# Kernel tuning notes

Hardware: AMD Instinct MI355X
Metric: run time of the kernel (lower is better)

## Reference

```python
import jax, jax.numpy as jnp
import numpy as np

N, E, IN, HID, OUT = 50000, 800000, 128, 96, 2


def setup_inputs() -> dict:
    key = jax.random.key(0)
    ks = jax.random.split(key, 10)
    x = jax.random.normal(ks[0], (N, IN), jnp.float32)
    edge_index = jax.random.randint(ks[1], (2, E), 0, N, dtype=jnp.int64)
    # PQVA mask: per-node, first output channel is a "known" quantity (masked out),
    # second is the prediction target -> ~mask selects exactly N elements.
    m = np.zeros((N, OUT), dtype=bool)
    m[:, 0] = True
    PQVA_mask = jnp.asarray(m)
    scaler_mean = 0.1 * jax.random.normal(ks[2], (IN,), jnp.float32)
    scaler_std = 0.5 + jax.random.uniform(ks[3], (IN,), jnp.float32)  # in [0.5, 1.5)
    W1 = jax.random.normal(ks[4], (IN, HID), jnp.float32) / np.sqrt(IN)
    W2 = jax.random.normal(ks[5], (HID, HID), jnp.float32) / np.sqrt(HID)
    W3 = jax.random.normal(ks[6], (HID, HID), jnp.float32) / np.sqrt(HID)
    Wout = jax.random.normal(ks[7], (HID, OUT), jnp.float32) / np.sqrt(HID)
    b1 = jnp.zeros((HID,), jnp.float32)
    b2 = jnp.zeros((HID,), jnp.float32)
    b3 = jnp.zeros((HID,), jnp.float32)
    bout = jnp.zeros((OUT,), jnp.float32)
    return {"x": x, "edge_index": edge_index, "PQVA_mask": PQVA_mask,
            "scaler_mean": scaler_mean, "scaler_std": scaler_std,
            "W1": W1, "b1": b1, "W2": W2, "b2": b2, "W3": W3, "b3": b3,
            "Wout": Wout, "bout": bout}


def reference(x, edge_index, PQVA_mask, scaler_mean, scaler_std,
              W1, b1, W2, b2, W3, b3, Wout, bout):
    n = x.shape[0]
    loop = jnp.arange(n, dtype=edge_index.dtype)
    src = jnp.concatenate([edge_index[0], loop])  # add self-loops (GCNConv default)
    dst = jnp.concatenate([edge_index[1], loop])
    deg = jax.ops.segment_sum(jnp.ones_like(dst, x.dtype), dst, num_segments=n)
    dinv = jax.lax.rsqrt(deg)  # deg >= 1 thanks to self-loops
    norm = (dinv[src] * dinv[dst])[:, None]  # [E+N, 1]

    def prop(h):  # D^-1/2 (A+I) D^-1/2 @ h  via gather-scale-scatter
        return jax.ops.segment_sum(h[src] * norm, dst, num_segments=n)

    h = (x - scaler_mean) / scaler_std          # standard scaler
    h = jax.nn.relu(prop(h @ W1) + b1)          # GCNConv 1 + ReLU
    h = jax.nn.relu(prop(h @ W2) + b2)          # GCNConv 2 + ReLU
    h = prop(h @ W3) + b3                       # GCNConv 3 (last, no act)
    out = h @ Wout + bout                       # final Linear -> [N, OUT]
    # masked reshape: ~mask has exactly one True per node -> [N]
    return out.reshape(-1)[~PQVA_mask.reshape(-1)]
```

## Files before the change

### kernel.cpp

```cpp
#include <hip/hip_runtime.h>
#include <hip/hip_fp16.h>

#define IN_F 128
#define HID_F 96
#define PB 512
#define STRIDE 6144
#define MAXB 8192

typedef _Float16 f16x8 __attribute__((ext_vector_type(8)));
typedef float f32x4 __attribute__((ext_vector_type(4)));

__device__ __forceinline__ void swizzle_one(const float* W, __half* Wsw, int idx) {
    int j  = idx & 7;
    int ln = (idx >> 3) & 63;
    int ct = idx >> 9;
    int t = ct % 6, c = ct / 6;
    int k   = c * 32 + (ln >> 4) * 8 + j;
    int col = t * 16 + (ln & 15);
    Wsw[idx] = (__half)W[k * 96 + col];
}


__global__ __launch_bounds__(256) void part_prep_kernel(
        const int* __restrict__ srcv, const int* __restrict__ dstv,
        int* __restrict__ bcur, int* __restrict__ ebuf, int E,
        const float* __restrict__ stdv, float* __restrict__ rstd,
        const float* __restrict__ W3, const float* __restrict__ Wout,
        const float* __restrict__ b3, const float* __restrict__ bout,
        float* __restrict__ wv, float* __restrict__ cconst,
        const float* __restrict__ W1, __half* __restrict__ Wsw1, int SW1,
        const float* __restrict__ W2, __half* __restrict__ Wsw2, int SW2) {
    int b = blockIdx.x, t = threadIdx.x;
    if (b >= PB) {
        int pb = b - PB;
        if (pb == 0) {
            if (t < IN_F) rstd[t] = 1.0f / stdv[t];
            if (t < HID_F) {
                float s = 0.f;
                for (int j = 0; j < HID_F; ++j) s += W3[t * HID_F + j] * Wout[j * 2 + 1];
                wv[t] = s;
            }
            if (t == 0) {
                float s = 0.f;
                for (int j = 0; j < HID_F; ++j) s += b3[j] * Wout[j * 2 + 1];
                cconst[0] = s + bout[1];
            }
        } else if (pb <= 48) {
            int idx = (pb - 1) * 256 + t;
            if (idx < SW1) swizzle_one(W1, Wsw1, idx);
        } else {
            int idx = (pb - 49) * 256 + t;
            if (idx < SW2) swizzle_one(W2, Wsw2, idx);
        }
        return;
    }
    __shared__ int h[256];
    __shared__ int cur[256];
    int chunk = (E + PB - 1) / PB;
    int s = b * chunk;
    int eend = min(s + chunk, E);
    h[t] = 0;
    __syncthreads();
    for (int e = s + t; e < eend; e += 256) atomicAdd(&h[dstv[e] >> 8], 1);
    __syncthreads();
    if (h[t]) cur[t] = t * STRIDE + atomicAdd(&bcur[t], h[t]);
    __syncthreads();
    for (int e = s + t; e < eend; e += 256) {
        int sv = srcv[e], d = dstv[e];
        int p = atomicAdd(&cur[d >> 8], 1);
        ebuf[p] = (sv << 8) | (d & 255);
    }
}


__global__ __launch_bounds__(256) void buildcsr_kernel(
        const int* __restrict__ ebuf, const int* __restrict__ bcur,
        int* __restrict__ rowdeg, float* __restrict__ dinv,
        int* __restrict__ cols, int n) {
    __shared__ int dg[256];
    __shared__ int tmp[256];
    __shared__ int cur[256];
    __shared__ int colst[MAXB];
    int t = threadIdx.x;
    int k = blockIdx.x;
    int seg = k * STRIDE;
    int cnt = min(bcur[k], STRIDE);
    dg[t] = 0;
    __syncthreads();
    for (int i = t; i < cnt; i += 256) atomicAdd(&dg[ebuf[seg + i] & 255], 1);
    __syncthreads();
    int v = dg[t];
    tmp[t] = v;
    __syncthreads();
#pragma unroll
    for (int off = 1; off < 256; off <<= 1) {
        int u = (t >= off) ? tmp[t - off] : 0;
        __syncthreads();
        tmp[t] += u;
        __syncthreads();
    }
    int excl = tmp[t] - v;
    int node = (k << 8) + t;
    if (node < n) {
        rowdeg[node] = ((seg + excl) << 9) | v;
        dinv[node] = rsqrtf((float)v + 1.0f);
    }
    cur[t] = excl;
    __syncthreads();
    for (int i = t; i < cnt; i += 256) {
        int p = ebuf[seg + i];
        int lp = atomicAdd(&cur[p & 255], 1);
        colst[lp] = ((unsigned)p) >> 8;
    }
    __syncthreads();
    for (int i = t; i < cnt; i += 256) cols[seg + i] = colst[i];
}


template<int MODE, int K>
__global__ __launch_bounds__(256) void gemm_mfma_kernel(
        const void* __restrict__ Ain, const __half* __restrict__ Wsw,
        const float* __restrict__ mean, const float* __restrict__ rstd,
        const float* __restrict__ dinv, __half* __restrict__ C, int n) {
    constexpr int NCH = K / 32;
    int lane = threadIdx.x & 63;
    int wv_  = threadIdx.x >> 6;
    int m = lane & 15, q = lane >> 4;
    int node0 = blockIdx.x * 64 + wv_ * 16;
    int g = node0 + m;
    int gc = g < n ? g : n - 1;

    f32x4 acc[6];
#pragma unroll
    for (int t = 0; t < 6; ++t) acc[t] = (f32x4){0.f, 0.f, 0.f, 0.f};

#pragma unroll
    for (int c = 0; c < NCH; ++c) {
        f16x8 a;
        if (MODE == 0) {
            const float* ap = (const float*)Ain + (long)gc * K + c * 32 + q * 8;
            float4 v0 = *(const float4*)ap;
            float4 v1 = *(const float4*)(ap + 4);
            float4 m0 = *(const float4*)(mean + c * 32 + q * 8);
            float4 m1 = *(const float4*)(mean + c * 32 + q * 8 + 4);
            float4 r0 = *(const float4*)(rstd + c * 32 + q * 8);
            float4 r1 = *(const float4*)(rstd + c * 32 + q * 8 + 4);
            a[0] = (_Float16)((v0.x - m0.x) * r0.x);
            a[1] = (_Float16)((v0.y - m0.y) * r0.y);
            a[2] = (_Float16)((v0.z - m0.z) * r0.z);
            a[3] = (_Float16)((v0.w - m0.w) * r0.w);
            a[4] = (_Float16)((v1.x - m1.x) * r1.x);
            a[5] = (_Float16)((v1.y - m1.y) * r1.y);
            a[6] = (_Float16)((v1.z - m1.z) * r1.z);
            a[7] = (_Float16)((v1.w - m1.w) * r1.w);
        } else {
            a = *(const f16x8*)((const __half*)Ain + (long)gc * K + c * 32 + q * 8);
        }
#pragma unroll
        for (int t = 0; t < 6; ++t) {
            f16x8 b = *(const f16x8*)(Wsw + (size_t)(((c * 6) + t) * 64 + lane) * 8);
            acc[t] = __builtin_amdgcn_mfma_f32_16x16x32_f16(a, b, acc[t], 0, 0, 0);
        }
    }
    float dv[4];
#pragma unroll
    for (int r = 0; r < 4; ++r) {
        int gr = node0 + q * 4 + r;
        dv[r] = (gr < n) ? dinv[gr] : 0.f;
    }
#pragma unroll
    for (int t = 0; t < 6; ++t)
#pragma unroll
        for (int r = 0; r < 4; ++r) {
            int gr = node0 + q * 4 + r;
            if (gr < n) C[(long)gr * 96 + t * 16 + m] = (__half)(acc[t][r] * dv[r]);
        }
}


template<int DOT>
__global__ __launch_bounds__(256) void prop16_kernel(
        const __half* __restrict__ hin, const int* __restrict__ rowdeg,
        const int* __restrict__ cols,
        const float* __restrict__ dinv, const float* __restrict__ bias,
        const float* __restrict__ wvv, __half* __restrict__ hout,
        float* __restrict__ zs, int n) {
    int wid = (blockIdx.x * blockDim.x + threadIdx.x) >> 6;
    int lane = threadIdx.x & 63;
    if (wid >= n) return;
    int rd = rowdeg[wid];
    int e0 = ((unsigned)rd) >> 9;
    int e1 = e0 + (rd & 511);
    bool active = lane < 48;
    int g = lane / 12, l = lane - g * 12;
    int gg = active ? g : 0;
    const f16x8* hp = (const f16x8*)hin;

    float acc[8];
#pragma unroll
    for (int j = 0; j < 8; ++j) acc[j] = 0.f;

    int e = e0;
    for (; e + 16 <= e1; e += 16) {
        int c0 = cols[e + gg];
        int c1 = cols[e + 4 + gg];
        int c2 = cols[e + 8 + gg];
        int c3 = cols[e + 12 + gg];
        f16x8 v0 = hp[(long)c0 * 12 + l];
        f16x8 v1 = hp[(long)c1 * 12 + l];
        f16x8 v2 = hp[(long)c2 * 12 + l];
        f16x8 v3 = hp[(long)c3 * 12 + l];
#pragma unroll
        for (int j = 0; j < 8; ++j)
            acc[j] += (float)v0[j] + (float)v1[j] + (float)v2[j] + (float)v3[j];
    }
    for (; e <= e1; e += 4) {
        int idx = e + gg;
        bool isedge = idx < e1;
        int c = wid;
        if (isedge) c = cols[idx];
        f16x8 v = hp[(long)c * 12 + l];
        float fm = (active && idx <= e1) ? 1.f : 0.f;
#pragma unroll
        for (int j = 0; j < 8; ++j) acc[j] += fm * (float)v[j];
    }
#pragma unroll
    for (int j = 0; j < 8; ++j) {
        acc[j] += __shfl_down(acc[j], 24, 64);
        acc[j] += __shfl_down(acc[j], 12, 64);
    }
    float di = dinv[wid];
    if (DOT == 0) {
        if (lane < 12) {
            float4 b0 = *(const float4*)(bias + lane * 8);
            float4 b1 = *(const float4*)(bias + lane * 8 + 4);
            f16x8 o;
            o[0] = (_Float16)fmaxf(di * acc[0] + b0.x, 0.f);
            o[1] = (_Float16)fmaxf(di * acc[1] + b0.y, 0.f);
            o[2] = (_Float16)fmaxf(di * acc[2] + b0.z, 0.f);
            o[3] = (_Float16)fmaxf(di * acc[3] + b0.w, 0.f);
            o[4] = (_Float16)fmaxf(di * acc[4] + b1.x, 0.f);
            o[5] = (_Float16)fmaxf(di * acc[5] + b1.y, 0.f);
            o[6] = (_Float16)fmaxf(di * acc[6] + b1.z, 0.f);
            o[7] = (_Float16)fmaxf(di * acc[7] + b1.w, 0.f);
            *(f16x8*)(hout + (long)wid * 96 + lane * 8) = o;
        }
    } else {
        float v = 0.f;
        if (lane < 12) {
            float4 b0 = *(const float4*)(bias + lane * 8);
            float4 b1 = *(const float4*)(bias + lane * 8 + 4);
            float4 w0 = *(const float4*)(wvv + lane * 8);
            float4 w1 = *(const float4*)(wvv + lane * 8 + 4);
            v  = fmaxf(di * acc[0] + b0.x, 0.f) * w0.x;
            v += fmaxf(di * acc[1] + b0.y, 0.f) * w0.y;
            v += fmaxf(di * acc[2] + b0.z, 0.f) * w0.z;
            v += fmaxf(di * acc[3] + b0.w, 0.f) * w0.w;
            v += fmaxf(di * acc[4] + b1.x, 0.f) * w1.x;
            v += fmaxf(di * acc[5] + b1.y, 0.f) * w1.y;
            v += fmaxf(di * acc[6] + b1.z, 0.f) * w1.z;
            v += fmaxf(di * acc[7] + b1.w, 0.f) * w1.w;
        }
#pragma unroll
        for (int off = 32; off; off >>= 1) v += __shfl_xor(v, off, 64);
        if (lane == 0) zs[wid] = di * v;
    }
}


__global__ __launch_bounds__(256) void prop_scalar_kernel(
        const float* __restrict__ zs, const int* __restrict__ rowdeg,
        const int* __restrict__ cols,
        const float* __restrict__ dinv, const float* __restrict__ cconst,
        float* __restrict__ out, int n) {
    int i = blockIdx.x * blockDim.x + threadIdx.x;
    if (i >= n) return;
    int rd = rowdeg[i];
    int e0 = ((unsigned)rd) >> 9;
    int e1 = e0 + (rd & 511);
    float s = 0.f;
    int e = e0;
    for (; e + 4 <= e1; e += 4) {
        int c0 = cols[e + 0], c1 = cols[e + 1], c2 = cols[e + 2], c3 = cols[e + 3];
        s += zs[c0]; s += zs[c1]; s += zs[c2]; s += zs[c3];
    }
    for (; e < e1; ++e) s += zs[cols[e]];
    out[i] = dinv[i] * (s + zs[i]) + cconst[0];
}


extern "C" void kernel_launch(void* const* d_in, const int* in_sizes, int n_in,
                              void* d_out, int out_size, void* d_ws, size_t ws_size,
                              hipStream_t stream) {
    const float* x    = (const float*)d_in[0];
    const int*   eidx = (const int*)d_in[1];
    const float* mean = (const float*)d_in[3];
    const float* stdv = (const float*)d_in[4];
    const float* W1   = (const float*)d_in[5];
    const float* b1   = (const float*)d_in[6];
    const float* W2   = (const float*)d_in[7];
    const float* b2   = (const float*)d_in[8];
    const float* W3   = (const float*)d_in[9];
    const float* b3   = (const float*)d_in[10];
    const float* Wout = (const float*)d_in[11];
    const float* bout = (const float*)d_in[12];
    float* out = (float*)d_out;

    const int n = in_sizes[0] / IN_F;
    const int E = in_sizes[1] / 2;
    const int* srcv = eidx;
    const int* dstv = eidx + E;
    const int NB = (n + 255) >> 8;

    char* ws = (char*)d_ws;
    size_t off = 0;
    auto alloc = [&](size_t bytes) -> void* {
        void* p = ws + off;
        off = (off + bytes + 255) & ~(size_t)255;
        return p;
    };
    const int SW1 = 4 * 6 * 64 * 8;
    const int SW2 = 3 * 6 * 64 * 8;
    int*    rowdeg = (int*)alloc((size_t)n * 4);
    float*  dinv   = (float*)alloc((size_t)n * 4);
    int*    cols   = (int*)alloc((size_t)256 * STRIDE * 4);
    int*    ebuf   = (int*)alloc((size_t)256 * STRIDE * 4);
    int*    bcur   = (int*)alloc(256 * 4);
    float*  rstd   = (float*)alloc(IN_F * 4);
    float*  wv     = (float*)alloc(HID_F * 4);
    float*  cconst = (float*)alloc(4);
    float*  zbuf   = (float*)alloc((size_t)n * 4);
    __half* Wsw1   = (__half*)alloc((size_t)SW1 * 2);
    __half* Wsw2   = (__half*)alloc((size_t)SW2 * 2);
    __half* bufA   = (__half*)alloc((size_t)n * HID_F * 2);
    __half* bufB   = (__half*)alloc((size_t)n * HID_F * 2);

    hipMemsetAsync(bcur, 0, 256 * 4, stream);

    part_prep_kernel<<<PB + 85, 256, 0, stream>>>(
        srcv, dstv, bcur, ebuf, E,
        stdv, rstd, W3, Wout, b3, bout, wv, cconst,
        W1, Wsw1, SW1, W2, Wsw2, SW2);
    buildcsr_kernel<<<NB, 256, 0, stream>>>(ebuf, bcur, rowdeg, dinv, cols, n);

    int gemm_grid = (n + 63) / 64;
    int prop_grid = (int)(((long)n * 64 + 255) / 256);

    gemm_mfma_kernel<0, IN_F><<<gemm_grid, 256, 0, stream>>>(x, Wsw1, mean, rstd, dinv,
                                                             bufA, n);
    prop16_kernel<0><<<prop_grid, 256, 0, stream>>>(bufA, rowdeg, cols, dinv, b1,
                                                    nullptr, bufB, nullptr, n);
    gemm_mfma_kernel<1, HID_F><<<gemm_grid, 256, 0, stream>>>(bufB, Wsw2, nullptr, nullptr,
                                                              dinv, bufA, n);
    prop16_kernel<1><<<prop_grid, 256, 0, stream>>>(bufA, rowdeg, cols, dinv, b2,
                                                    wv, nullptr, zbuf, n);
    prop_scalar_kernel<<<(n + 255) / 256, 256, 0, stream>>>(zbuf, rowdeg, cols, dinv,
                                                            cconst, out, n);
}
```

Measured before the change: 211.9 us.

## Split hidden features into 32-column blocks and propagate per block

The GEMM output and propagation buffers change from node-major 96-wide rows to three column-blocked planes, each 32 halfs wide per node. Propagation now launches one pass per column block, so each pass gathers from a smaller feature plane that should sit better in cache. Each wave handles one node with 16 edges per step and 4 lanes per row. The final dot-product stage adds per-block partial sums with atomics into a zeroed buffer, and the dinv scaling moves into the scalar propagation. The cost is three times as many waves, fewer independent gathers in flight per wave per iteration, and extra atomics.

```diff
diff --git a/kernel.cpp b/kernel.cpp
--- a/kernel.cpp
+++ b/kernel.cpp
@@ -19,7 +19,6 @@
     int col = t * 16 + (ln & 15);
     Wsw[idx] = (__half)W[k * 96 + col];
 }
-
 
 __global__ __launch_bounds__(256) void part_prep_kernel(
         const int* __restrict__ srcv, const int* __restrict__ dstv,
@@ -72,7 +71,6 @@
     }
 }
 
-
 __global__ __launch_bounds__(256) void buildcsr_kernel(
         const int* __restrict__ ebuf, const int* __restrict__ bcur,
         int* __restrict__ rowdeg, float* __restrict__ dinv,
@@ -154,7 +152,7 @@
             a[6] = (_Float16)((v1.z - m1.z) * r1.z);
             a[7] = (_Float16)((v1.w - m1.w) * r1.w);
         } else {
-            a = *(const f16x8*)((const __half*)Ain + (long)gc * K + c * 32 + q * 8);
+            a = *(const f16x8*)((const __half*)Ain + ((size_t)c * n + gc) * 32 + q * 8);
         }
 #pragma unroll
         for (int t = 0; t < 6; ++t) {
@@ -169,32 +167,36 @@
         dv[r] = (gr < n) ? dinv[gr] : 0.f;
     }
 #pragma unroll
-    for (int t = 0; t < 6; ++t)
+    for (int t = 0; t < 6; ++t) {
+        int cb = t >> 1;
+        int co = (t & 1) * 16 + m;
 #pragma unroll
         for (int r = 0; r < 4; ++r) {
             int gr = node0 + q * 4 + r;
-            if (gr < n) C[(long)gr * 96 + t * 16 + m] = (__half)(acc[t][r] * dv[r]);
-        }
+            if (gr < n) C[((size_t)cb * n + gr) * 32 + co] = (__half)(acc[t][r] * dv[r]);
+        }
+    }
 }
 
 
 template<int DOT>
-__global__ __launch_bounds__(256) void prop16_kernel(
+__global__ __launch_bounds__(256) void prop32_kernel(
         const __half* __restrict__ hin, const int* __restrict__ rowdeg,
         const int* __restrict__ cols,
         const float* __restrict__ dinv, const float* __restrict__ bias,
         const float* __restrict__ wvv, __half* __restrict__ hout,
-        float* __restrict__ zs, int n) {
-    int wid = (blockIdx.x * blockDim.x + threadIdx.x) >> 6;
+        float* __restrict__ zacc, int n, int bpp) {
+    int wv_  = threadIdx.x >> 6;
     int lane = threadIdx.x & 63;
-    if (wid >= n) return;
-    int rd = rowdeg[wid];
+    int cb = blockIdx.x / bpp;
+    int nb = blockIdx.x - cb * bpp;
+    int node = nb * 4 + wv_;
+    if (node >= n) return;
+    int rd = rowdeg[node];
     int e0 = ((unsigned)rd) >> 9;
     int e1 = e0 + (rd & 511);
-    bool active = lane < 48;
-    int g = lane / 12, l = lane - g * 12;
-    int gg = active ? g : 0;
-    const f16x8* hp = (const f16x8*)hin;
+    int g = lane >> 2, l = lane & 3;
+    const f16x8* hp = (const f16x8*)hin + (size_t)cb * n * 4 + l;
 
     float acc[8];
 #pragma unroll
@@ -202,38 +204,33 @@
 
     int e = e0;
     for (; e + 16 <= e1; e += 16) {
-        int c0 = cols[e + gg];
-        int c1 = cols[e + 4 + gg];
-        int c2 = cols[e + 8 + gg];
-        int c3 = cols[e + 12 + gg];
-        f16x8 v0 = hp[(long)c0 * 12 + l];
-        f16x8 v1 = hp[(long)c1 * 12 + l];
-        f16x8 v2 = hp[(long)c2 * 12 + l];
-        f16x8 v3 = hp[(long)c3 * 12 + l];
-#pragma unroll
-        for (int j = 0; j < 8; ++j)
-            acc[j] += (float)v0[j] + (float)v1[j] + (float)v2[j] + (float)v3[j];
-    }
-    for (; e <= e1; e += 4) {
-        int idx = e + gg;
+        int c = cols[e + g];
+        f16x8 v = hp[(size_t)c * 4];
+#pragma unroll
+        for (int j = 0; j < 8; ++j) acc[j] += (float)v[j];
+    }
+    {
+        int idx = e + g;
         bool isedge = idx < e1;
-        int c = wid;
-        if (isedge) c = cols[idx];
-        f16x8 v = hp[(long)c * 12 + l];
-        float fm = (active && idx <= e1) ? 1.f : 0.f;
+        int c = isedge ? cols[idx] : node;
+        f16x8 v = hp[(size_t)c * 4];
+        float fm = (idx <= e1) ? 1.f : 0.f;
 #pragma unroll
         for (int j = 0; j < 8; ++j) acc[j] += fm * (float)v[j];
     }
 #pragma unroll
     for (int j = 0; j < 8; ++j) {
-        acc[j] += __shfl_down(acc[j], 24, 64);
-        acc[j] += __shfl_down(acc[j], 12, 64);
-    }
-    float di = dinv[wid];
+        acc[j] += __shfl_down(acc[j], 32, 64);
+        acc[j] += __shfl_down(acc[j], 16, 64);
+        acc[j] += __shfl_down(acc[j],  8, 64);
+        acc[j] += __shfl_down(acc[j],  4, 64);
+    }
+    float di = dinv[node];
     if (DOT == 0) {
-        if (lane < 12) {
-            float4 b0 = *(const float4*)(bias + lane * 8);
-            float4 b1 = *(const float4*)(bias + lane * 8 + 4);
+        if (lane < 4) {
+            const float* bp = bias + cb * 32 + lane * 8;
+            float4 b0 = *(const float4*)bp;
+            float4 b1 = *(const float4*)(bp + 4);
             f16x8 o;
             o[0] = (_Float16)fmaxf(di * acc[0] + b0.x, 0.f);
             o[1] = (_Float16)fmaxf(di * acc[1] + b0.y, 0.f);
@@ -243,15 +240,17 @@
             o[5] = (_Float16)fmaxf(di * acc[5] + b1.y, 0.f);
             o[6] = (_Float16)fmaxf(di * acc[6] + b1.z, 0.f);
             o[7] = (_Float16)fmaxf(di * acc[7] + b1.w, 0.f);
-            *(f16x8*)(hout + (long)wid * 96 + lane * 8) = o;
+            *(f16x8*)(hout + ((size_t)cb * n + node) * 32 + lane * 8) = o;
         }
     } else {
         float v = 0.f;
-        if (lane < 12) {
-            float4 b0 = *(const float4*)(bias + lane * 8);
-            float4 b1 = *(const float4*)(bias + lane * 8 + 4);
-            float4 w0 = *(const float4*)(wvv + lane * 8);
-            float4 w1 = *(const float4*)(wvv + lane * 8 + 4);
+        if (lane < 4) {
+            const float* bp = bias + cb * 32 + lane * 8;
+            const float* wp = wvv  + cb * 32 + lane * 8;
+            float4 b0 = *(const float4*)bp;
+            float4 b1 = *(const float4*)(bp + 4);
+            float4 w0 = *(const float4*)wp;
+            float4 w1 = *(const float4*)(wp + 4);
             v  = fmaxf(di * acc[0] + b0.x, 0.f) * w0.x;
             v += fmaxf(di * acc[1] + b0.y, 0.f) * w0.y;
             v += fmaxf(di * acc[2] + b0.z, 0.f) * w0.z;
@@ -261,15 +260,15 @@
             v += fmaxf(di * acc[6] + b1.z, 0.f) * w1.z;
             v += fmaxf(di * acc[7] + b1.w, 0.f) * w1.w;
         }
-#pragma unroll
-        for (int off = 32; off; off >>= 1) v += __shfl_xor(v, off, 64);
-        if (lane == 0) zs[wid] = di * v;
+        v += __shfl_xor(v, 1, 64);
+        v += __shfl_xor(v, 2, 64);
+        if (lane == 0) atomicAdd(zacc + node, v);
     }
 }
 
 
 __global__ __launch_bounds__(256) void prop_scalar_kernel(
-        const float* __restrict__ zs, const int* __restrict__ rowdeg,
+        const float* __restrict__ zacc, const int* __restrict__ rowdeg,
         const int* __restrict__ cols,
         const float* __restrict__ dinv, const float* __restrict__ cconst,
         float* __restrict__ out, int n) {
@@ -282,10 +281,14 @@
     int e = e0;
     for (; e + 4 <= e1; e += 4) {
         int c0 = cols[e + 0], c1 = cols[e + 1], c2 = cols[e + 2], c3 = cols[e + 3];
-        s += zs[c0]; s += zs[c1]; s += zs[c2]; s += zs[c3];
-    }
-    for (; e < e1; ++e) s += zs[cols[e]];
-    out[i] = dinv[i] * (s + zs[i]) + cconst[0];
+        s += dinv[c0] * zacc[c0];
+        s += dinv[c1] * zacc[c1];
+        s += dinv[c2] * zacc[c2];
+        s += dinv[c3] * zacc[c3];
+    }
+    for (; e < e1; ++e) { int c = cols[e]; s += dinv[c] * zacc[c]; }
+    float di = dinv[i];
+    out[i] = di * (s + di * zacc[i]) + cconst[0];
 }
 
 
@@ -326,16 +329,16 @@
     int*    cols   = (int*)alloc((size_t)256 * STRIDE * 4);
     int*    ebuf   = (int*)alloc((size_t)256 * STRIDE * 4);
     int*    bcur   = (int*)alloc(256 * 4);
+    float*  zsacc  = (float*)alloc((size_t)n * 4);
     float*  rstd   = (float*)alloc(IN_F * 4);
     float*  wv     = (float*)alloc(HID_F * 4);
     float*  cconst = (float*)alloc(4);
-    float*  zbuf   = (float*)alloc((size_t)n * 4);
     __half* Wsw1   = (__half*)alloc((size_t)SW1 * 2);
     __half* Wsw2   = (__half*)alloc((size_t)SW2 * 2);
     __half* bufA   = (__half*)alloc((size_t)n * HID_F * 2);
     __half* bufB   = (__half*)alloc((size_t)n * HID_F * 2);
 
-    hipMemsetAsync(bcur, 0, 256 * 4, stream);
+    hipMemsetAsync(bcur, 0, 1024 + (size_t)n * 4, stream);
 
     part_prep_kernel<<<PB + 85, 256, 0, stream>>>(
         srcv, dstv, bcur, ebuf, E,
@@ -344,16 +347,16 @@
     buildcsr_kernel<<<NB, 256, 0, stream>>>(ebuf, bcur, rowdeg, dinv, cols, n);
 
     int gemm_grid = (n + 63) / 64;
-    int prop_grid = (int)(((long)n * 64 + 255) / 256);
+    int bpp = (n + 3) / 4;
 
     gemm_mfma_kernel<0, IN_F><<<gemm_grid, 256, 0, stream>>>(x, Wsw1, mean, rstd, dinv,
                                                              bufA, n);
-    prop16_kernel<0><<<prop_grid, 256, 0, stream>>>(bufA, rowdeg, cols, dinv, b1,
-                                                    nullptr, bufB, nullptr, n);
+    prop32_kernel<0><<<3 * bpp, 256, 0, stream>>>(bufA, rowdeg, cols, dinv, b1,
+                                                  nullptr, bufB, nullptr, n, bpp);
     gemm_mfma_kernel<1, HID_F><<<gemm_grid, 256, 0, stream>>>(bufB, Wsw2, nullptr, nullptr,
                                                               dinv, bufA, n);
-    prop16_kernel<1><<<prop_grid, 256, 0, stream>>>(bufA, rowdeg, cols, dinv, b2,
-                                                    wv, nullptr, zbuf, n);
-    prop_scalar_kernel<<<(n + 255) / 256, 256, 0, stream>>>(zbuf, rowdeg, cols, dinv,
+    prop32_kernel<1><<<3 * bpp, 256, 0, stream>>>(bufA, rowdeg, cols, dinv, b2,
+                                                  wv, nullptr, zsacc, n, bpp);
+    prop_scalar_kernel<<<(n + 255) / 256, 256, 0, stream>>>(zsacc, rowdeg, cols, dinv,
                                                             cconst, out, n);
 }
```

Measured after the change: 265.7 us. 25.4% more time.

## Fuse CSR build with first GEMM and preload neighbor columns via shuffles

Applied to the files above, without the earlier changes.

Merges the CSR-building kernel and the first feature GEMM into one launch by giving extra blocks the GEMM work, which removes a launch and lets the two independent stages run concurrently. The first GEMM no longer scales by dinv, so the first propagation instead gathers dinv for each neighbor and multiplies it in. The propagation kernel also loads up to 64 column indices with a single coalesced load per wave and distributes them with shuffles, handles the self-loop separately, and only reads further indices from memory for high-degree nodes. The cost is an extra per-edge dinv gather in layer 1 and more complex control flow.

```diff
diff --git a/kernel.cpp b/kernel.cpp
--- a/kernel.cpp
+++ b/kernel.cpp
@@ -19,7 +19,6 @@
     int col = t * 16 + (ln & 15);
     Wsw[idx] = (__half)W[k * 96 + col];
 }
-
 
 __global__ __launch_bounds__(256) void part_prep_kernel(
         const int* __restrict__ srcv, const int* __restrict__ dstv,
@@ -73,60 +72,17 @@
 }
 
 
-__global__ __launch_bounds__(256) void buildcsr_kernel(
-        const int* __restrict__ ebuf, const int* __restrict__ bcur,
-        int* __restrict__ rowdeg, float* __restrict__ dinv,
-        int* __restrict__ cols, int n) {
-    __shared__ int dg[256];
-    __shared__ int tmp[256];
-    __shared__ int cur[256];
-    __shared__ int colst[MAXB];
-    int t = threadIdx.x;
-    int k = blockIdx.x;
-    int seg = k * STRIDE;
-    int cnt = min(bcur[k], STRIDE);
-    dg[t] = 0;
-    __syncthreads();
-    for (int i = t; i < cnt; i += 256) atomicAdd(&dg[ebuf[seg + i] & 255], 1);
-    __syncthreads();
-    int v = dg[t];
-    tmp[t] = v;
-    __syncthreads();
-#pragma unroll
-    for (int off = 1; off < 256; off <<= 1) {
-        int u = (t >= off) ? tmp[t - off] : 0;
-        __syncthreads();
-        tmp[t] += u;
-        __syncthreads();
-    }
-    int excl = tmp[t] - v;
-    int node = (k << 8) + t;
-    if (node < n) {
-        rowdeg[node] = ((seg + excl) << 9) | v;
-        dinv[node] = rsqrtf((float)v + 1.0f);
-    }
-    cur[t] = excl;
-    __syncthreads();
-    for (int i = t; i < cnt; i += 256) {
-        int p = ebuf[seg + i];
-        int lp = atomicAdd(&cur[p & 255], 1);
-        colst[lp] = ((unsigned)p) >> 8;
-    }
-    __syncthreads();
-    for (int i = t; i < cnt; i += 256) cols[seg + i] = colst[i];
-}
-
-
-template<int MODE, int K>
-__global__ __launch_bounds__(256) void gemm_mfma_kernel(
+template<int MODE, int K, int SC>
+__device__ __forceinline__ void gemm_body(
+        int bid, int tid,
         const void* __restrict__ Ain, const __half* __restrict__ Wsw,
         const float* __restrict__ mean, const float* __restrict__ rstd,
         const float* __restrict__ dinv, __half* __restrict__ C, int n) {
     constexpr int NCH = K / 32;
-    int lane = threadIdx.x & 63;
-    int wv_  = threadIdx.x >> 6;
+    int lane = tid & 63;
+    int wv_  = tid >> 6;
     int m = lane & 15, q = lane >> 4;
-    int node0 = blockIdx.x * 64 + wv_ * 16;
+    int node0 = bid * 64 + wv_ * 16;
     int g = node0 + m;
     int gc = g < n ? g : n - 1;
 
@@ -166,19 +122,79 @@
 #pragma unroll
     for (int r = 0; r < 4; ++r) {
         int gr = node0 + q * 4 + r;
-        dv[r] = (gr < n) ? dinv[gr] : 0.f;
+        dv[r] = SC ? ((gr < n) ? dinv[gr] : 0.f) : 1.f;
     }
 #pragma unroll
     for (int t = 0; t < 6; ++t)
 #pragma unroll
         for (int r = 0; r < 4; ++r) {
             int gr = node0 + q * 4 + r;
-            if (gr < n) C[(long)gr * 96 + t * 16 + m] = (__half)(acc[t][r] * dv[r]);
-        }
-}
-
-
-template<int DOT>
+            float o = SC ? acc[t][r] * dv[r] : acc[t][r];
+            if (gr < n) C[(long)gr * 96 + t * 16 + m] = (__half)o;
+        }
+}
+
+template<int MODE, int K, int SC>
+__global__ __launch_bounds__(256) void gemm_mfma_kernel(
+        const void* __restrict__ Ain, const __half* __restrict__ Wsw,
+        const float* __restrict__ mean, const float* __restrict__ rstd,
+        const float* __restrict__ dinv, __half* __restrict__ C, int n) {
+    gemm_body<MODE, K, SC>(blockIdx.x, threadIdx.x, Ain, Wsw, mean, rstd, dinv, C, n);
+}
+
+
+__global__ __launch_bounds__(256) void csr_gemm1_kernel(
+        const int* __restrict__ ebuf, const int* __restrict__ bcur,
+        int* __restrict__ rowdeg, float* __restrict__ dinv,
+        int* __restrict__ cols, int n, int nb,
+        const float* __restrict__ x, const __half* __restrict__ Wsw1,
+        const float* __restrict__ mean, const float* __restrict__ rstd,
+        __half* __restrict__ C) {
+    __shared__ int dg[256];
+    __shared__ int tmp[256];
+    __shared__ int cur[256];
+    __shared__ int colst[MAXB];
+    int t = threadIdx.x;
+    if (blockIdx.x >= nb) {
+        gemm_body<0, IN_F, 0>(blockIdx.x - nb, t, x, Wsw1, mean, rstd, nullptr, C, n);
+        return;
+    }
+    int k = blockIdx.x;
+    int seg = k * STRIDE;
+    int cnt = min(bcur[k], STRIDE);
+    dg[t] = 0;
+    __syncthreads();
+    for (int i = t; i < cnt; i += 256) atomicAdd(&dg[ebuf[seg + i] & 255], 1);
+    __syncthreads();
+    int v = dg[t];
+    tmp[t] = v;
+    __syncthreads();
+#pragma unroll
+    for (int off = 1; off < 256; off <<= 1) {
+        int u = (t >= off) ? tmp[t - off] : 0;
+        __syncthreads();
+        tmp[t] += u;
+        __syncthreads();
+    }
+    int excl = tmp[t] - v;
+    int node = (k << 8) + t;
+    if (node < n) {
+        rowdeg[node] = ((seg + excl) << 9) | v;
+        dinv[node] = rsqrtf((float)v + 1.0f);
+    }
+    cur[t] = excl;
+    __syncthreads();
+    for (int i = t; i < cnt; i += 256) {
+        int p = ebuf[seg + i];
+        int lp = atomicAdd(&cur[p & 255], 1);
+        colst[lp] = ((unsigned)p) >> 8;
+    }
+    __syncthreads();
+    for (int i = t; i < cnt; i += 256) cols[seg + i] = colst[i];
+}
+
+
+template<int DOT, int SCALE>
 __global__ __launch_bounds__(256) void prop16_kernel(
         const __half* __restrict__ hin, const int* __restrict__ rowdeg,
         const int* __restrict__ cols,
@@ -190,46 +206,69 @@
     if (wid >= n) return;
     int rd = rowdeg[wid];
     int e0 = ((unsigned)rd) >> 9;
-    int e1 = e0 + (rd & 511);
+    int deg = rd & 511;
+    float di = dinv[wid];
     bool active = lane < 48;
     int g = lane / 12, l = lane - g * 12;
     int gg = active ? g : 0;
     const f16x8* hp = (const f16x8*)hin;
 
+    int colv = cols[e0 + lane];
+    f16x8 vself = hp[(long)wid * 12 + l];
+
     float acc[8];
-#pragma unroll
-    for (int j = 0; j < 8; ++j) acc[j] = 0.f;
-
-    int e = e0;
-    for (; e + 16 <= e1; e += 16) {
-        int c0 = cols[e + gg];
-        int c1 = cols[e + 4 + gg];
-        int c2 = cols[e + 8 + gg];
-        int c3 = cols[e + 12 + gg];
+    float sself = (g == 0) ? (SCALE ? di : 1.f) : 0.f;
+#pragma unroll
+    for (int j = 0; j < 8; ++j) acc[j] = sself * (float)vself[j];
+
+    int dcap = deg < 64 ? deg : 64;
+    int e = 0;
+    for (; e + 16 <= dcap; e += 16) {
+        int p = e + gg;
+        int c0 = __shfl(colv, p, 64);
+        int c1 = __shfl(colv, p + 4, 64);
+        int c2 = __shfl(colv, p + 8, 64);
+        int c3 = __shfl(colv, p + 12, 64);
+        float s0 = 1.f, s1 = 1.f, s2 = 1.f, s3 = 1.f;
+        if (SCALE) { s0 = dinv[c0]; s1 = dinv[c1]; s2 = dinv[c2]; s3 = dinv[c3]; }
         f16x8 v0 = hp[(long)c0 * 12 + l];
         f16x8 v1 = hp[(long)c1 * 12 + l];
         f16x8 v2 = hp[(long)c2 * 12 + l];
         f16x8 v3 = hp[(long)c3 * 12 + l];
 #pragma unroll
-        for (int j = 0; j < 8; ++j)
-            acc[j] += (float)v0[j] + (float)v1[j] + (float)v2[j] + (float)v3[j];
-    }
-    for (; e <= e1; e += 4) {
+        for (int j = 0; j < 8; ++j) {
+            acc[j] = fmaf((float)v0[j], s0, acc[j]);
+            acc[j] = fmaf((float)v1[j], s1, acc[j]);
+            acc[j] = fmaf((float)v2[j], s2, acc[j]);
+            acc[j] = fmaf((float)v3[j], s3, acc[j]);
+        }
+    }
+    for (; e < dcap; e += 4) {
         int idx = e + gg;
-        bool isedge = idx < e1;
-        int c = wid;
-        if (isedge) c = cols[idx];
+        bool is = active && idx < dcap;
+        int cs = __shfl(colv, idx & 63, 64);
+        int c = is ? cs : wid;
         f16x8 v = hp[(long)c * 12 + l];
-        float fm = (active && idx <= e1) ? 1.f : 0.f;
-#pragma unroll
-        for (int j = 0; j < 8; ++j) acc[j] += fm * (float)v[j];
+        float sc = SCALE ? dinv[c] : 1.f;
+        float s = is ? sc : 0.f;
+#pragma unroll
+        for (int j = 0; j < 8; ++j) acc[j] = fmaf((float)v[j], s, acc[j]);
+    }
+    for (int ee = 64; ee < deg; ee += 4) {
+        int idx = ee + gg;
+        bool is = active && idx < deg;
+        int c = is ? cols[e0 + idx] : wid;
+        f16x8 v = hp[(long)c * 12 + l];
+        float sc = SCALE ? dinv[c] : 1.f;
+        float s = is ? sc : 0.f;
+#pragma unroll
+        for (int j = 0; j < 8; ++j) acc[j] = fmaf((float)v[j], s, acc[j]);
     }
 #pragma unroll
     for (int j = 0; j < 8; ++j) {
         acc[j] += __shfl_down(acc[j], 24, 64);
         acc[j] += __shfl_down(acc[j], 12, 64);
     }
-    float di = dinv[wid];
     if (DOT == 0) {
         if (lane < 12) {
             float4 b0 = *(const float4*)(bias + lane * 8);
@@ -341,19 +380,19 @@
         srcv, dstv, bcur, ebuf, E,
         stdv, rstd, W3, Wout, b3, bout, wv, cconst,
         W1, Wsw1, SW1, W2, Wsw2, SW2);
-    buildcsr_kernel<<<NB, 256, 0, stream>>>(ebuf, bcur, rowdeg, dinv, cols, n);
 
     int gemm_grid = (n + 63) / 64;
     int prop_grid = (int)(((long)n * 64 + 255) / 256);
 
-    gemm_mfma_kernel<0, IN_F><<<gemm_grid, 256, 0, stream>>>(x, Wsw1, mean, rstd, dinv,
-                                                             bufA, n);
-    prop16_kernel<0><<<prop_grid, 256, 0, stream>>>(bufA, rowdeg, cols, dinv, b1,
-                                                    nullptr, bufB, nullptr, n);
-    gemm_mfma_kernel<1, HID_F><<<gemm_grid, 256, 0, stream>>>(bufB, Wsw2, nullptr, nullptr,
-                                                              dinv, bufA, n);
-    prop16_kernel<1><<<prop_grid, 256, 0, stream>>>(bufA, rowdeg, cols, dinv, b2,
-                                                    wv, nullptr, zbuf, n);
+    csr_gemm1_kernel<<<NB + gemm_grid, 256, 0, stream>>>(
+        ebuf, bcur, rowdeg, dinv, cols, n, NB, x, Wsw1, mean, rstd, bufA);
+
+    prop16_kernel<0, 1><<<prop_grid, 256, 0, stream>>>(bufA, rowdeg, cols, dinv, b1,
+                                                       nullptr, bufB, nullptr, n);
+    gemm_mfma_kernel<1, HID_F, 1><<<gemm_grid, 256, 0, stream>>>(
+        bufB, Wsw2, nullptr, nullptr, dinv, bufA, n);
+    prop16_kernel<1, 0><<<prop_grid, 256, 0, stream>>>(bufA, rowdeg, cols, dinv, b2,
+                                                       wv, nullptr, zbuf, n);
     prop_scalar_kernel<<<(n + 255) / 256, 256, 0, stream>>>(zbuf, rowdeg, cols, dinv,
                                                             cconst, out, n);
 }
```

Result: faster. 200.6 us (-5.4%).
